# Kernel optimization log

Hardware: AMD Instinct MI355X
Metric: run time of the kernel (lower is better)

The kernel has to match this reference:

```python
import jax, jax.numpy as jnp
import numpy as np

# dims
B, H, W = 2, 128, 256
MD = 34            # model_dim (last 2 channels = sin/cos lat)
LD = MD - 2        # learnable_dim = 32
NH, HD = 4, 8      # n_heads, head_dim
SH = 64            # shared_hidden (DISCO out channels)
K = 25             # number of DISCO basis functions (5x5 kernel_shape)
P = 7              # local stencil width (lat x lon support of geodesic basis)
R = P // 2
FF1, FF2 = 512, 256


def setup_inputs() -> dict:
    key = jax.random.key(0)
    ks = jax.random.split(key, 16)
    x = jax.random.normal(ks[0], (B, H, W, MD), dtype=jnp.float32)
    # latitude-dependent sparse geodesic basis values over a 7x7 stencil
    psi_val = jax.random.uniform(ks[1], (K, H, P * P), dtype=jnp.float32) * 0.1
    disco_w = jax.random.normal(ks[2], (SH, K), dtype=jnp.float32) * 0.1
    disco_b = jax.random.normal(ks[3], (SH,), dtype=jnp.float32) * 0.01
    # per-head MLP: shared_hidden -> 32 -> 1
    hw1 = jax.random.normal(ks[4], (NH, SH, 32), dtype=jnp.float32) * (1.0 / np.sqrt(SH))
    hb1 = jax.random.normal(ks[5], (NH, 32), dtype=jnp.float32) * 0.01
    hw2 = jax.random.normal(ks[6], (NH, 32, 1), dtype=jnp.float32) * (1.0 / np.sqrt(32))
    hb2 = jax.random.normal(ks[7], (NH, 1), dtype=jnp.float32) * 0.01
    # FFN: model_dim -> 512 -> 256 -> learnable_dim
    fw1 = jax.random.normal(ks[8], (MD, FF1), dtype=jnp.float32) * (1.0 / np.sqrt(MD))
    fw1 = fw1.at[-2:, :].set(0.0)  # matches ffn[0].weight[:, -2:] = 0 init
    fb1 = jax.random.normal(ks[9], (FF1,), dtype=jnp.float32) * 0.01
    fw2 = jax.random.normal(ks[10], (FF1, FF2), dtype=jnp.float32) * (1.0 / np.sqrt(FF1))
    fb2 = jax.random.normal(ks[11], (FF2,), dtype=jnp.float32) * 0.01
    fw3 = jax.random.normal(ks[12], (FF2, LD), dtype=jnp.float32) * (1.0 / np.sqrt(FF2))
    fb3 = jax.random.normal(ks[13], (LD,), dtype=jnp.float32) * 0.01
    return {"x": x, "psi_val": psi_val, "disco_w": disco_w, "disco_b": disco_b,
            "hw1": hw1, "hb1": hb1, "hw2": hw2, "hb2": hb2,
            "fw1": fw1, "fb1": fb1, "fw2": fw2, "fb2": fb2, "fw3": fw3, "fb3": fb3}


def _gelu(t):
    return jax.nn.gelu(t, approximate=False)  # torch nn.GELU default (erf)


def _disco_s2(xn, psi_val, disco_w, disco_b):
    """DISCO sparse-basis conv on single-channel maps.
    xn: (N, H, W). Basis values vary with output latitude, longitude is
    translation-invariant; support is a lat-clamped / lon-wrapped 7x7 stencil.
    Returns (N, SH, H, W)."""
    xp = jnp.pad(xn, ((0, 0), (R, R), (0, 0)), mode="edge")  # clamp at poles
    shifts = []
    for dlat in range(P):
        row = xp[:, dlat:dlat + H, :]
        for dlon in range(-R, R + 1):
            shifts.append(jnp.roll(row, -dlon, axis=2))  # wrap in longitude
    xs = jnp.stack(shifts, axis=1)  # (N, P*P, H, W)
    basis = jnp.einsum("khp,nphw->nkhw", psi_val, xs)       # basis aggregation
    return jnp.einsum("fk,nkhw->nfhw", disco_w, basis) + disco_b[None, :, None, None]


def reference(x, psi_val, disco_w, disco_b, hw1, hb1, hw2, hb2,
              fw1, fb1, fw2, fb2, fw3, fb3):
    x_learn = x[..., :LD]
    sin_cos = x[..., LD:]
    x_res = x_learn
    # (B,H,W,LD) -> (B*LD, H, W): each learnable channel is a 1-channel map
    xn = x_learn.transpose(0, 3, 1, 2).reshape(B * LD, H, W)
    d = _disco_s2(xn, psi_val, disco_w, disco_b)              # (B*LD, SH, H, W)
    d = d.reshape(B, LD, SH, H, W).transpose(0, 3, 4, 1, 2)    # (B,H,W,LD,SH)
    # per-head MLP over its head_dim slice (head index is outer in LD)
    d = d.reshape(B, H, W, NH, HD, SH)
    h = _gelu(jnp.einsum("bxynds,nso->bxyndo", d, hw1) + hb1[None, None, None, :, None, :])
    h = jnp.einsum("bxyndo,noe->bxynde", h, hw2) + hb2[None, None, None, :, None, :]
    x_learn = h[..., 0].reshape(B, H, W, LD)
    x_learn = x_learn + x_res                                  # use_residual
    x_full = jnp.concatenate([x_learn, sin_cos], axis=-1)
    x_res2 = x_learn
    t = _gelu(x_full @ fw1 + fb1)
    t = _gelu(t @ fw2 + fb2)
    t = t @ fw3 + fb3                                          # dropout p=0 -> id
    x_learn = t + x_res2
    return jnp.concatenate([x_learn, sin_cos], axis=-1)
```

## Files before the change

### kernel.cpp

```cpp
#include <hip/hip_runtime.h>
#include <math.h>


typedef __attribute__((ext_vector_type(8))) short bfrag;
typedef __attribute__((ext_vector_type(4))) float ffrag;
typedef __attribute__((ext_vector_type(4))) short short4v;

union bfi4 { int4 i; bfrag b; };

__device__ __forceinline__ float gelu_f(float v) {
  const float z = v * (2.3022077484f + 0.1029451564f * v * v);
  const float e = __builtin_amdgcn_exp2f(-z);
  return v * __builtin_amdgcn_rcpf(1.0f + e);
}

__device__ __forceinline__ short f2bf(float f) {
  union { float f; unsigned u; } v; v.f = f;
  unsigned r = (v.u + 0x7fffu + ((v.u >> 16) & 1u)) >> 16;
  return (short)r;
}

__device__ __forceinline__ short f2bf_fast(float f) {
  union { float f; unsigned u; } v; v.f = f;
  return (short)((v.u + 0x8000u) >> 16);
}

__device__ __forceinline__ float bf2f(short s) {
  union { float f; unsigned u; } v;
  v.u = ((unsigned)(unsigned short)s) << 16;
  return v.f;
}

template <int CTRL>
__device__ __forceinline__ float dpp_add(float v) {
  union { float f; int i; } s, t;
  s.f = v;
  t.i = __builtin_amdgcn_update_dpp(0, s.i, CTRL, 0xf, 0xf, true);
  return v + t.f;
}
__device__ __forceinline__ float reduce16(float v) {
  v = dpp_add<0xB1>(v);
  v = dpp_add<0x4E>(v);
  v = dpp_add<0x141>(v);
  v = dpp_add<0x140>(v);
  return v;
}

__device__ __forceinline__ void st4bf(short* p, float4 v) {
  short4v s;
  s[0] = f2bf(v.x); s[1] = f2bf(v.y); s[2] = f2bf(v.z); s[3] = f2bf(v.w);
  *(short4v*)p = s;
}

__device__ __forceinline__ void tile_map(int& w0, int& b, int& h, int& lin) {
  lin  = blockIdx.x + (blockIdx.y << 3) + (blockIdx.z << 10);
  const int xcd  = lin & 7;
  const int slot = lin >> 3;
  w0 = (slot & 7) * 32;
  b  = (slot >> 3) & 1;
  h  = (xcd << 4) | (slot >> 4);
}

__global__ __launch_bounds__(256) void k01_prep(
    const float* __restrict__ psi, const float* __restrict__ dw,
    const float* __restrict__ db,
    const float* __restrict__ fw1, const float* __restrict__ fw2,
    const float* __restrict__ fw3, const float* __restrict__ hw1,
    const float* __restrict__ hb1,
    short* __restrict__ wcb, short* __restrict__ fw1s,
    short* __restrict__ fw2s, short* __restrict__ fw3s,
    float* __restrict__ hb1e) {
  __shared__ __align__(16) char sm[24832];
  const int bid = blockIdx.x;
  const int tid = threadIdx.x;

  if (bid < 512) {
    float* tileL = (float*)sm;
    float* hw1n  = (float*)(sm + 13312);
    short* tile2 = (short*)(sm + 21504);
    const int h = bid >> 2;
    const int n = bid & 3;
    const int lane = tid & 63;
    const int w = __builtin_amdgcn_readfirstlane(tid >> 6);

    for (int e = tid; e < 512; e += 256)
      ((float4*)hw1n)[e] = ((const float4*)(hw1 + n * 2048))[e];

    float dwreg[25];
#pragma unroll
    for (int kk = 0; kk < 25; ++kk) dwreg[kk] = dw[lane * 25 + kk];
    const int p0 = w * 13;
    const int pend = (p0 + 13 < 49) ? (p0 + 13) : 49;
#pragma unroll 1
    for (int p = p0; p < pend; ++p) {
      float acc = 0.f;
#pragma unroll
      for (int kk = 0; kk < 25; ++kk)
        acc += dwreg[kk] * psi[kk * 6272 + h * 49 + p];
      tileL[lane * 52 + p] = acc;
    }
    __syncthreads();

    const int o = tid & 31;
#pragma unroll 1
    for (int pp = tid >> 5; pp < 25; pp += 8) {
      const int p2 = pp * 2;
      float a0 = 0.f, a1 = 0.f;
#pragma unroll 4
      for (int f = 0; f < 64; ++f) {
        const float wv = hw1n[f * 32 + o];
        a0 += wv * tileL[f * 52 + p2];
        a1 += wv * tileL[f * 52 + p2 + 1];
      }
      tile2[o * 52 + p2] = f2bf(a0);
      if (p2 + 1 < 49) tile2[o * 52 + p2 + 1] = f2bf(a1);
    }
    __syncthreads();

    short* outp = wcb + h * 16384 + n * 4096;
    for (int idx = tid; idx < 4096; idx += 256) {
      const int jj = idx & 7, ln = (idx >> 3) & 63;
      const int nt = (idx >> 9) & 1, kt = (idx >> 10) & 1;
      const int par = idx >> 11;
      const int k = kt * 32 + ((ln >> 4) << 3) + jj;
      const int oo = nt * 16 + (ln & 15);
      const int r = k >> 3, dlt = k & 7;
      const int j = par ? (dlt - 1) : dlt;
      short v = 0;
      if (r < 7 && j >= 0 && j < 7) v = tile2[oo * 52 + r * 7 + j];
      outp[idx] = v;
    }
    return;
  }

  if (bid < 528) {
    short* S = (short*)sm;
    const int kt = bid - 512;
    const float* src = fw2 + kt * 8192;
    for (int q = tid; q < 2048; q += 256) {
      const int lin = q * 4;
      const int kk = lin >> 8, nn = lin & 255;
      st4bf(S + kk * 260 + nn, *(const float4*)(src + lin));
    }
    __syncthreads();
    short* dst = fw2s + kt * 8192;
    for (int q = tid; q < 8192; q += 256) {
      const int jj = q & 7, lane = (q >> 3) & 63, nt = q >> 9;
      const int kk = (lane >> 4) * 8 + jj, nn = nt * 16 + (lane & 15);
      dst[q] = S[kk * 260 + nn];
    }
    return;
  }

  if (bid < 530) {
    const int X = bid - 528;
    short* S = (short*)sm;
    for (int q = tid; q < 2048; q += 256) {
      const int lin = q * 4;
      const int kk = lin >> 8, nn = lin & 255;
      st4bf(S + kk * 260 + nn, *(const float4*)(fw1 + kk * 512 + X * 256 + nn));
    }
    __syncthreads();
    for (int q = tid; q < 8192; q += 256) {
      const int jj = q & 7, lane = (q >> 3) & 63, ntl = q >> 9;
      const int kk = (lane >> 4) * 8 + jj, nn = ntl * 16 + (lane & 15);
      fw1s[X * 8192 + q] = S[kk * 260 + nn];
    }
    return;
  }

  if (bid == 530) {
    short* S = (short*)sm;
    for (int q = tid; q < 2048; q += 256) {
      const int lin = q * 4;
      const int kk = lin >> 5, nn = lin & 31;
      st4bf(S + kk * 36 + nn, *(const float4*)(fw3 + lin));
    }
    __syncthreads();
    for (int q = tid; q < 8192; q += 256) {
      const int jj = q & 7, lane = (q >> 3) & 63;
      const int nt = (q >> 9) & 1, kt = q >> 10;
      const int kk = kt * 32 + (lane >> 4) * 8 + jj, nn = nt * 16 + (lane & 15);
      fw3s[q] = S[kk * 36 + nn];
    }
    return;
  }

  if (tid < 128) {
    const int n = tid >> 5, o = tid & 31;
    float acc = hb1[n * 32 + o];
#pragma unroll
    for (int s = 0; s < 64; ++s)
      acc += hw1[n * 2048 + s * 32 + o] * db[s];
    hb1e[tid] = acc;
  }
}

__global__ __launch_bounds__(256, 8) void k2_conv(
    const float* __restrict__ x,    const short* __restrict__ wcb,
    const float* __restrict__ hb1e, const float* __restrict__ hw2,
    const float* __restrict__ hb2,  short* __restrict__ wsM) {
  __shared__ __align__(16) char smem[20384];
  short* sX = (short*)smem;
  short* sM = (short*)(smem + 18080);

  const int tid = threadIdx.x;
  int w0, b, h, lin;
  tile_map(w0, b, h, lin);

  const int lane = tid & 63, lm = lane & 15, lq = lane >> 4;
  const int n = tid >> 6;

  float hb1v[2], hw2v[2];
#pragma unroll
  for (int nt = 0; nt < 2; ++nt) {
    hb1v[nt] = hb1e[n * 32 + nt * 16 + lm];
    hw2v[nt] = hw2[n * 32 + nt * 16 + lm];
  }
  const float hb2n = hb2[n];

  {
    int4* p = (int4*)smem;
    int4 z; z.x = z.y = z.z = z.w = 0;
    for (int e = tid; e < 20384 / 16; e += 256) p[e] = z;
  }
  __syncthreads();

#pragma unroll 1
  for (int r = 0; r < 7; ++r) {
    int hr = h - 3 + r; hr = hr < 0 ? 0 : (hr > 127 ? 127 : hr);
    const float* __restrict__ xrow = x + (size_t)((b * 128 + hr) * 256) * 34;
    short* __restrict__ sxr = sX + r * 40;
    for (int e = tid; e < 39 * 16; e += 256) {
      const int c2 = e & 15;
      const int wp = e >> 4;
      const int wr = (w0 - 3 + wp) & 255;
      const float2 v = *(const float2*)&xrow[wr * 34 + c2 * 2];
      short* dp = sxr + (c2 * 2) * 280 + wp;
      dp[0]   = f2bf_fast(v.x);
      dp[280] = f2bf_fast(v.y);
    }
  }
  __syncthreads();

  const int* tpB = (const int*)sX;

#pragma unroll 1
  for (int par = 0; par < 2; ++par) {
    bfrag cw[2][2];
#pragma unroll
    for (int kt = 0; kt < 2; ++kt)
#pragma unroll
      for (int nt = 0; nt < 2; ++nt)
        cw[kt][nt] = *(const bfrag*)(wcb + h * 16384 + n * 4096 +
                         ((par * 2 + kt) * 2 + nt) * 512 + lane * 8);

#pragma unroll 1
    for (int i = 0; i < 8; ++i) {
      const int c = n * 8 + i;

      const int base0 = c * 140 + lq * 20 + lm;
      bfi4 u0, u1;
      u0.i.x = tpB[base0];      u0.i.y = tpB[base0 + 1];
      u0.i.z = tpB[base0 + 2];  u0.i.w = tpB[base0 + 3];
      u1.i.x = tpB[base0 + 80]; u1.i.y = tpB[base0 + 81];
      u1.i.z = tpB[base0 + 82]; u1.i.w = tpB[base0 + 83];

      ffrag h0 = {0.f, 0.f, 0.f, 0.f}, h1 = {0.f, 0.f, 0.f, 0.f};
      h0 = __builtin_amdgcn_mfma_f32_16x16x32_bf16(u0.b, cw[0][0], h0, 0, 0, 0);
      h0 = __builtin_amdgcn_mfma_f32_16x16x32_bf16(u1.b, cw[1][0], h0, 0, 0, 0);
      h1 = __builtin_amdgcn_mfma_f32_16x16x32_bf16(u0.b, cw[0][1], h1, 0, 0, 0);
      h1 = __builtin_amdgcn_mfma_f32_16x16x32_bf16(u1.b, cw[1][1], h1, 0, 0, 0);

#pragma unroll
      for (int rr = 0; rr < 4; ++rr) {
        float v = gelu_f(h0[rr] + hb1v[0]) * hw2v[0] +
                  gelu_f(h1[rr] + hb1v[1]) * hw2v[1];
        v = reduce16(v);
        const int p = 2 * (lq * 4 + rr) + par;
        const float res = bf2f(sX[c * 280 + 123 + p]);
        if (lm == 0) sM[p * 36 + c] = f2bf_fast(v + hb2n + res);
      }
    }
  }
  __syncthreads();

  {
    const int row = tid >> 3, c4 = (tid & 7) * 4;
    *(short4v*)(wsM + lin * 1024 + tid * 4) = *(const short4v*)(sM + row * 36 + c4);
  }
}

__global__ __launch_bounds__(256, 8) void k3_mlp(
    const float* __restrict__ x,    const short* __restrict__ wsM,
    const short* __restrict__ fw1s, const short* __restrict__ fw2s,
    const short* __restrict__ fw3s,
    const float* __restrict__ fb1,  const float* __restrict__ fb2,
    const float* __restrict__ fb3,  float* __restrict__ outb) {
  __shared__ __align__(16) char smem[19200];
  short* sT1h = (short*)smem;
  short* sT2  = (short*)smem;
  float* sO   = (float*)smem;
  short* sMv  = (short*)(smem + 16896);

  const int tid = threadIdx.x;
  int w0, b, h, lin;
  tile_map(w0, b, h, lin);

  const int lane = tid & 63, lm = lane & 15, lq = lane >> 4;
  const int wave = tid >> 6;
  const int koff = lq * 8;

  {
    const int row = tid >> 3, c4 = (tid & 7) * 4;
    *(short4v*)(sMv + row * 36 + c4) = *(const short4v*)(wsM + lin * 1024 + tid * 4);
  }
  __syncthreads();

  const int mt3 = wave & 1;
  const int nt3 = wave >> 1;
  const int col3 = nt3 * 16 + lm;
  const int pixg = (b * 128 + h) * 256 + w0;
  const int n0 = wave * 4;

  ffrag acc[2][4];
#pragma unroll
  for (int mt = 0; mt < 2; ++mt)
#pragma unroll
    for (int ni = 0; ni < 4; ++ni) acc[mt][ni] = ffrag{0.f, 0.f, 0.f, 0.f};
  const short* w2base = fw2s + n0 * 512 + lane * 8;

#pragma unroll 1
  for (int H = 0; H < 2; ++H) {
#pragma unroll
    for (int ni = 0; ni < 4; ++ni) {
      const bfrag b1f = *(const bfrag*)(fw1s +
                          (H * 16 + wave * 4 + ni) * 512 + lane * 8);
      const int ntl = wave * 4 + ni;
#pragma unroll
      for (int mt = 0; mt < 2; ++mt) {
        const bfrag aFm = *(const bfrag*)(sMv + (mt * 16 + lm) * 36 + koff);
        ffrag cc = {0.f, 0.f, 0.f, 0.f};
        cc = __builtin_amdgcn_mfma_f32_16x16x32_bf16(aFm, b1f, cc, 0, 0, 0);
        const float bias = fb1[H * 256 + ntl * 16 + lm];
#pragma unroll
        for (int r = 0; r < 4; ++r) {
          const int row = mt * 16 + lq * 4 + r;
          sT1h[row * 264 + ntl * 16 + lm] = f2bf_fast(gelu_f(cc[r] + bias));
        }
      }
    }
    __syncthreads();

#pragma unroll 1
    for (int kt = 0; kt < 8; ++kt) {
      const bfrag a0 = *(const bfrag*)(sT1h + lm * 264 + kt * 32 + koff);
      const bfrag a1 = *(const bfrag*)(sT1h + (16 + lm) * 264 + kt * 32 + koff);
#pragma unroll
      for (int np = 0; np < 2; ++np) {
        const bfrag bv0 = *(const bfrag*)(w2base + (H * 8 + kt) * 8192 + (2 * np) * 512);
        const bfrag bv1 = *(const bfrag*)(w2base + (H * 8 + kt) * 8192 + (2 * np + 1) * 512);
        acc[0][2 * np]     = __builtin_amdgcn_mfma_f32_16x16x32_bf16(a0, bv0, acc[0][2 * np], 0, 0, 0);
        acc[1][2 * np]     = __builtin_amdgcn_mfma_f32_16x16x32_bf16(a1, bv0, acc[1][2 * np], 0, 0, 0);
        acc[0][2 * np + 1] = __builtin_amdgcn_mfma_f32_16x16x32_bf16(a0, bv1, acc[0][2 * np + 1], 0, 0, 0);
        acc[1][2 * np + 1] = __builtin_amdgcn_mfma_f32_16x16x32_bf16(a1, bv1, acc[1][2 * np + 1], 0, 0, 0);
      }
    }
    __syncthreads();
  }

#pragma unroll
  for (int mt = 0; mt < 2; ++mt)
#pragma unroll
    for (int ni = 0; ni < 4; ++ni) {
      const int col = (n0 + ni) * 16 + lm;
      const float bias = fb2[col];
#pragma unroll
      for (int r = 0; r < 4; ++r) {
        const int row = mt * 16 + lq * 4 + r;
        sT2[row * 264 + col] = f2bf_fast(gelu_f(acc[mt][ni][r] + bias));
      }
    }
  __syncthreads();

  ffrag c3 = {0.f, 0.f, 0.f, 0.f};
  const short* sA3 = sT2 + (mt3 * 16 + lm) * 264 + koff;
#pragma unroll
  for (int kt = 0; kt < 8; ++kt) {
    const bfrag a = *(const bfrag*)(sA3 + kt * 32);
    const bfrag bw = *(const bfrag*)(fw3s + nt3 * 512 + kt * 1024 + lane * 8);
    c3 = __builtin_amdgcn_mfma_f32_16x16x32_bf16(a, bw, c3, 0, 0, 0);
  }
  __syncthreads();
  {
    const float bias = fb3[col3];
#pragma unroll
    for (int r = 0; r < 4; ++r) {
      const int row = mt3 * 16 + lq * 4 + r;
      const float res = bf2f(sMv[row * 36 + col3]);
      sO[row * 34 + col3] = c3[r] + bias + res;
    }
  }
  if (tid < 32) {
    const float2 scv =
        *(const float2*)&x[(size_t)(((b * 128 + h) * 256 + w0 + tid)) * 34 + 32];
    sO[tid * 34 + 32] = scv.x;
    sO[tid * 34 + 33] = scv.y;
  }
  __syncthreads();
  {
    const float4* sp = (const float4*)sO;
    float4* dp = (float4*)(outb + (size_t)pixg * 34);
    for (int e = tid; e < 272; e += 256) dp[e] = sp[e];
  }
}

extern "C" void kernel_launch(void* const* d_in, const int* in_sizes, int n_in,
                              void* d_out, int out_size, void* d_ws, size_t ws_size,
                              hipStream_t stream) {
  const float* x   = (const float*)d_in[0];
  const float* psi = (const float*)d_in[1];
  const float* dw  = (const float*)d_in[2];
  const float* db  = (const float*)d_in[3];
  const float* hw1 = (const float*)d_in[4];
  const float* hb1 = (const float*)d_in[5];
  const float* hw2 = (const float*)d_in[6];
  const float* hb2 = (const float*)d_in[7];
  const float* fw1 = (const float*)d_in[8];
  const float* fb1 = (const float*)d_in[9];
  const float* fw2 = (const float*)d_in[10];
  const float* fb2 = (const float*)d_in[11];
  const float* fw3 = (const float*)d_in[12];
  const float* fb3 = (const float*)d_in[13];
  float* outb = (float*)d_out;

  short* wcb  = (short*)d_ws;
  short* fw1s = wcb + 2097152;
  short* fw2s = fw1s + 16384;
  short* fw3s = fw2s + 131072;
  float* hb1e = (float*)(fw3s + 8192);
  short* wsM  = (short*)(hb1e + 128);

  hipLaunchKernelGGL(k01_prep, dim3(532), dim3(256), 0, stream,
                     psi, dw, db, fw1, fw2, fw3, hw1, hb1,
                     wcb, fw1s, fw2s, fw3s, hb1e);
  hipLaunchKernelGGL(k2_conv, dim3(8, 128, 2), dim3(256), 0, stream,
                     x, wcb, hb1e, hw2, hb2, wsM);
  hipLaunchKernelGGL(k3_mlp, dim3(8, 128, 2), dim3(256), 0, stream,
                     x, wsM, fw1s, fw2s, fw3s, fb1, fb2, fb3, outb);
}
```

Baseline: 168.8 us.

## Fuse DISCO conv/head-MLP kernel with FFN kernel into one launch

Merges k2_conv and k3_mlp into a single kernel, k23_fused. The per-tile bf16 activation matrix now stays in shared memory (sM) and feeds the FFN directly, instead of going out to a global workspace and being read back. This removes one kernel launch, the global write and read of the intermediate, and a sync. The FFN scratch buffers reuse the conv's shared-memory region below sM. The risk is higher register pressure in the combined kernel, which could lower occupancy.

```diff
diff --git a/kernel.cpp b/kernel.cpp
--- a/kernel.cpp
+++ b/kernel.cpp
@@ -196,10 +196,14 @@
   }
 }
 
-__global__ __launch_bounds__(256, 8) void k2_conv(
+__global__ __launch_bounds__(256, 8) void k23_fused(
     const float* __restrict__ x,    const short* __restrict__ wcb,
     const float* __restrict__ hb1e, const float* __restrict__ hw2,
-    const float* __restrict__ hb2,  short* __restrict__ wsM) {
+    const float* __restrict__ hb2,
+    const short* __restrict__ fw1s, const short* __restrict__ fw2s,
+    const short* __restrict__ fw3s,
+    const float* __restrict__ fb1,  const float* __restrict__ fb2,
+    const float* __restrict__ fb3,  float* __restrict__ outb) {
   __shared__ __align__(16) char smem[20384];
   short* sX = (short*)smem;
   short* sM = (short*)(smem + 18080);
@@ -285,38 +289,11 @@
   }
   __syncthreads();
 
-  {
-    const int row = tid >> 3, c4 = (tid & 7) * 4;
-    *(short4v*)(wsM + lin * 1024 + tid * 4) = *(const short4v*)(sM + row * 36 + c4);
-  }
-}
-
-__global__ __launch_bounds__(256, 8) void k3_mlp(
-    const float* __restrict__ x,    const short* __restrict__ wsM,
-    const short* __restrict__ fw1s, const short* __restrict__ fw2s,
-    const short* __restrict__ fw3s,
-    const float* __restrict__ fb1,  const float* __restrict__ fb2,
-    const float* __restrict__ fb3,  float* __restrict__ outb) {
-  __shared__ __align__(16) char smem[19200];
   short* sT1h = (short*)smem;
   short* sT2  = (short*)smem;
   float* sO   = (float*)smem;
-  short* sMv  = (short*)(smem + 16896);
-
-  const int tid = threadIdx.x;
-  int w0, b, h, lin;
-  tile_map(w0, b, h, lin);
-
-  const int lane = tid & 63, lm = lane & 15, lq = lane >> 4;
-  const int wave = tid >> 6;
+  const int wave = n;
   const int koff = lq * 8;
-
-  {
-    const int row = tid >> 3, c4 = (tid & 7) * 4;
-    *(short4v*)(sMv + row * 36 + c4) = *(const short4v*)(wsM + lin * 1024 + tid * 4);
-  }
-  __syncthreads();
-
   const int mt3 = wave & 1;
   const int nt3 = wave >> 1;
   const int col3 = nt3 * 16 + lm;
@@ -339,7 +316,7 @@
       const int ntl = wave * 4 + ni;
 #pragma unroll
       for (int mt = 0; mt < 2; ++mt) {
-        const bfrag aFm = *(const bfrag*)(sMv + (mt * 16 + lm) * 36 + koff);
+        const bfrag aFm = *(const bfrag*)(sM + (mt * 16 + lm) * 36 + koff);
         ffrag cc = {0.f, 0.f, 0.f, 0.f};
         cc = __builtin_amdgcn_mfma_f32_16x16x32_bf16(aFm, b1f, cc, 0, 0, 0);
         const float bias = fb1[H * 256 + ntl * 16 + lm];
@@ -397,7 +374,7 @@
 #pragma unroll
     for (int r = 0; r < 4; ++r) {
       const int row = mt3 * 16 + lq * 4 + r;
-      const float res = bf2f(sMv[row * 36 + col3]);
+      const float res = bf2f(sM[row * 36 + col3]);
       sO[row * 34 + col3] = c3[r] + bias + res;
     }
   }
@@ -439,13 +416,11 @@
   short* fw2s = fw1s + 16384;
   short* fw3s = fw2s + 131072;
   float* hb1e = (float*)(fw3s + 8192);
-  short* wsM  = (short*)(hb1e + 128);
 
   hipLaunchKernelGGL(k01_prep, dim3(532), dim3(256), 0, stream,
                      psi, dw, db, fw1, fw2, fw3, hw1, hb1,
                      wcb, fw1s, fw2s, fw3s, hb1e);
-  hipLaunchKernelGGL(k2_conv, dim3(8, 128, 2), dim3(256), 0, stream,
-                     x, wcb, hb1e, hw2, hb2, wsM);
-  hipLaunchKernelGGL(k3_mlp, dim3(8, 128, 2), dim3(256), 0, stream,
-                     x, wsM, fw1s, fw2s, fw3s, fb1, fb2, fb3, outb);
-}
+  hipLaunchKernelGGL(k23_fused, dim3(8, 128, 2), dim3(256), 0, stream,
+                     x, wcb, hb1e, hw2, hb2,
+                     fw1s, fw2s, fw3s, fb1, fb2, fb3, outb);
+}
```

Result: no change. 166.3 us (-1.5%).
